# Kernel optimization log

Hardware: AMD Instinct MI355X
Metric: run time of the kernel (lower is better)

The kernel has to match this reference:

```python
import jax, jax.numpy as jnp
import numpy as np

N = 50000      # nodes
E = 800000     # edges (before self loops)
IN = 128       # in_channels
H = 8          # heads
C = 32         # hidden_channels per head
HC = H * C     # 256, concat head dim
G = 256        # number of graphs
NEG_SLOPE = 0.2  # PyG GATConv default


def gat_conv(h_in, src, dst, W, att_s, att_d, bias):
    """PyG-style GATConv, concat heads. src/dst include self loops.
    h_in: [N, F_in]; W: [H*C, F_in]; att_s/att_d: [H, C]; bias: [H*C]."""
    h = (h_in @ W.T).reshape(N, H, C)                      # [N,H,C]
    a_s = jnp.sum(h * att_s, axis=-1)                      # [N,H]
    a_d = jnp.sum(h * att_d, axis=-1)                      # [N,H]
    e = jax.nn.leaky_relu(a_s[src] + a_d[dst], NEG_SLOPE)  # [E',H]
    # segment softmax over incoming edges of each dst node
    m = jax.ops.segment_max(e, dst, num_segments=N)        # [N,H]
    p = jnp.exp(e - m[dst])                                # [E',H]
    denom = jax.ops.segment_sum(p, dst, num_segments=N)    # [N,H]
    alpha = p / denom[dst]                                 # [E',H]
    msg = alpha[:, :, None] * h[src]                       # [E',H,C]
    out = jax.ops.segment_sum(msg, dst, num_segments=N)    # [N,H,C]
    return out.reshape(N, HC) + bias


def setup_inputs() -> dict:
    key = jax.random.key(0)
    ks = jax.random.split(key, 20)
    s = 0.1
    inp = {
        "x": jax.random.normal(ks[0], (N, IN), jnp.float32),
        "edge_index": jax.random.randint(ks[1], (2, E), 0, N, dtype=jnp.int64),
        "batch": jnp.sort(jax.random.randint(ks[2], (N,), 0, G, dtype=jnp.int64)),
        # layer 1: IN -> H*C
        "W1": jax.random.normal(ks[3], (HC, IN), jnp.float32) * s,
        "as1": jax.random.normal(ks[4], (H, C), jnp.float32) * s,
        "ad1": jax.random.normal(ks[5], (H, C), jnp.float32) * s,
        "b1": jnp.zeros((HC,), jnp.float32),
        # layer 2: H*C -> H*C
        "W2": jax.random.normal(ks[6], (HC, HC), jnp.float32) * s,
        "as2": jax.random.normal(ks[7], (H, C), jnp.float32) * s,
        "ad2": jax.random.normal(ks[8], (H, C), jnp.float32) * s,
        "b2": jnp.zeros((HC,), jnp.float32),
        # layer 3: H*C -> H*C
        "W3": jax.random.normal(ks[9], (HC, HC), jnp.float32) * s,
        "as3": jax.random.normal(ks[10], (H, C), jnp.float32) * s,
        "ad3": jax.random.normal(ks[11], (H, C), jnp.float32) * s,
        "b3": jnp.zeros((HC,), jnp.float32),
        # final linear H*C -> 1
        "Wf": jax.random.normal(ks[12], (1, HC), jnp.float32) * s,
        "bf": jnp.zeros((1,), jnp.float32),
    }
    return inp


def reference(x, edge_index, batch, W1, as1, ad1, b1, W2, as2, ad2, b2,
              W3, as3, ad3, b3, Wf, bf):
    # add self loops once (PyG GATConv default add_self_loops=True)
    loop = jnp.arange(N, dtype=edge_index.dtype)
    src = jnp.concatenate([edge_index[0], loop])
    dst = jnp.concatenate([edge_index[1], loop])

    h = jax.nn.relu(gat_conv(x, src, dst, W1, as1, ad1, b1))
    # dropout p=0.01, eval mode -> identity
    h = jax.nn.relu(gat_conv(h, src, dst, W2, as2, ad2, b2))
    h = gat_conv(h, src, dst, W3, as3, ad3, b3)

    # global mean pool per graph
    sums = jax.ops.segment_sum(h, batch, num_segments=G)          # [G,HC]
    cnt = jax.ops.segment_sum(jnp.ones((N, 1), h.dtype), batch, num_segments=G)
    pooled = sums / jnp.maximum(cnt, 1.0)                         # [G,HC]
    return pooled @ Wf.T + bf                                     # [G,1]
```

## Files before the change

kernel.cpp:

```cpp
#include <hip/hip_runtime.h>

#define N_NODES 50000
#define E_EDGES 800000
#define E_EXT   850000
#define IN_CH   128
#define HC      256
#define NHEAD   8
#define CH      32
#define NGRAPH  256
#define SCAN_CHUNK 1024
#define N_CHUNKS ((N_NODES + SCAN_CHUNK - 1) / SCAN_CHUNK)

typedef __bf16 bf16x8 __attribute__((ext_vector_type(8)));
typedef float  f32x4  __attribute__((ext_vector_type(4)));

__device__ inline ushort f2bf(float f) {
    union { float f; unsigned u; } v; v.f = f;
    unsigned u = v.u;
    unsigned r = u + 0x7FFFu + ((u >> 16) & 1u);
    return (ushort)(r >> 16);
}
__device__ inline float bflo(unsigned u) {
    union { unsigned u; float f; } v; v.u = u << 16; return v.f;
}
__device__ inline float bfhi(unsigned u) {
    union { unsigned u; float f; } v; v.u = u & 0xFFFF0000u; return v.f;
}

#define W1_N4 (HC * IN_CH / 4)
#define W23_N4 (HC * HC / 4)
#define CVT_N4 (W1_N4 + 2 * W23_N4)
#define V1_N  (32 * IN_CH)
#define V23_N (32 * HC)
#define COMP_TOT (V1_N + 2 * V23_N)
#define PREP_TOT (CVT_N4 + COMP_TOT + E_EXT)
__global__ __launch_bounds__(256) void prep_kernel(
    const float* __restrict__ W1, const float* __restrict__ W2,
    const float* __restrict__ W3,
    ushort* __restrict__ W1b, ushort* __restrict__ W2b, ushort* __restrict__ W3b,
    const float* __restrict__ as1, const float* __restrict__ ad1,
    const float* __restrict__ as2, const float* __restrict__ ad2,
    const float* __restrict__ as3, const float* __restrict__ ad3,
    const float* __restrict__ b3, const float* __restrict__ Wf,
    float* __restrict__ bw,
    ushort* __restrict__ Vb1, ushort* __restrict__ Vb2, ushort* __restrict__ Vb3,
    const int* __restrict__ ei, int* __restrict__ deg)
{
    int i = blockIdx.x * blockDim.x + threadIdx.x;
    if (blockIdx.x == 0 && threadIdx.x < NHEAD) {
        float s = 0.f;
        for (int c = 0; c < CH; c++)
            s += b3[threadIdx.x * CH + c] * Wf[threadIdx.x * CH + c];
        bw[threadIdx.x] = s;
    }
    if (i < CVT_N4) {
        const float* src; ushort* dst; int k;
        if (i < W1_N4) { src = W1; dst = W1b; k = i; }
        else if (i < W1_N4 + W23_N4) { src = W2; dst = W2b; k = i - W1_N4; }
        else { src = W3; dst = W3b; k = i - W1_N4 - W23_N4; }
        float4 v = *(const float4*)(src + (size_t)k * 4);
        ushort4 o;
        o.x = f2bf(v.x); o.y = f2bf(v.y); o.z = f2bf(v.z); o.w = f2bf(v.w);
        *(ushort4*)(dst + (size_t)k * 4) = o;
        return;
    }
    int c2 = i - CVT_N4;
    if (c2 < COMP_TOT) {
        const float* Wsrc; const float* aw; ushort* dst; int F_, j, k;
        int nrows;
        if (c2 < V1_N) {
            F_ = IN_CH; j = c2 >> 7; k = c2 & 127; Wsrc = W1; dst = Vb1;
            aw = (j < 8) ? as1 : ad1; nrows = 16;
        } else if (c2 < V1_N + V23_N) {
            c2 -= V1_N;
            F_ = HC; j = c2 >> 8; k = c2 & 255; Wsrc = W2; dst = Vb2;
            aw = (j < 8) ? as2 : ad2; nrows = 16;
        } else {
            c2 -= V1_N + V23_N;
            F_ = HC; j = c2 >> 8; k = c2 & 255; Wsrc = W3; dst = Vb3;
            aw = (j < 8) ? as3 : (j < 16 ? Wf : ad3); nrows = 24;
        }
        float v = 0.f;
        if (j < nrows) {
            int h = j & 7;
            for (int c = 0; c < CH; c++)
                v += aw[h * CH + c] * Wsrc[(size_t)(h * CH + c) * F_ + k];
        }
        dst[j * F_ + k] = f2bf(v);
        return;
    }
    int e = i - CVT_N4 - COMP_TOT;
    if (e < E_EXT) {
        int d = (e < E_EDGES) ? ei[E_EDGES + e] : (e - E_EDGES);
        atomicAdd(&deg[d], 1);
    }
}

__global__ __launch_bounds__(256) void mfma_gemm_kernel(
    const ushort* __restrict__ Xb, const float* __restrict__ Xf,
    const ushort* __restrict__ Wb, const ushort* __restrict__ Vb,
    ushort* __restrict__ Hb, int M, int F,
    float* __restrict__ as_out, float* __restrict__ ad_out)
{
    __shared__ ushort As[128][40];
    __shared__ ushort Bs[128][40];
    __shared__ ushort Vs[16][40];
    const int tid  = threadIdx.x;
    const int lane = tid & 63;
    const int wave = tid >> 6;
    const int wr = (wave >> 1) * 64;
    const int wc = (wave & 1) * 64;
    const int bm = blockIdx.x * 128;
    const int bn = blockIdx.y * 128;
    const int lrow = tid >> 2;
    const int lseg = (tid & 3) * 8;
    const int fr = lane & 15;
    const int fk = (lane >> 4) * 8;
    const bool doV = (Vb != nullptr) && (blockIdx.y == 0) && !(wave & 1);

    f32x4 zero = {0.f, 0.f, 0.f, 0.f};
    f32x4 acc[4][4];
    f32x4 accv[4];
    #pragma unroll
    for (int i = 0; i < 4; i++) {
        accv[i] = zero;
        #pragma unroll
        for (int j = 0; j < 4; j++) acc[i][j] = zero;
    }

    for (int k0 = 0; k0 < F; k0 += 32) {
        #pragma unroll
        for (int rr = 0; rr < 2; rr++) {
            int row = lrow + rr * 64;
            int arow = bm + row;
            bf16x8 av = {};
            if (Xf) {
                if (arow < M) {
                    float4 lo = *(const float4*)(Xf + (size_t)arow * F + k0 + lseg);
                    float4 hi = *(const float4*)(Xf + (size_t)arow * F + k0 + lseg + 4);
                    ushort t[8] = { f2bf(lo.x), f2bf(lo.y), f2bf(lo.z), f2bf(lo.w),
                                    f2bf(hi.x), f2bf(hi.y), f2bf(hi.z), f2bf(hi.w) };
                    av = *(const bf16x8*)t;
                }
            } else {
                if (arow < M) av = *(const bf16x8*)(Xb + (size_t)arow * F + k0 + lseg);
            }
            *(bf16x8*)(&As[row][lseg]) = av;
            bf16x8 bv = *(const bf16x8*)(Wb + (size_t)(bn + row) * F + k0 + lseg);
            *(bf16x8*)(&Bs[row][lseg]) = bv;
        }
        if (Vb && tid < 64) {
            int vr = tid >> 2;
            *(bf16x8*)(&Vs[vr][lseg]) = *(const bf16x8*)(Vb + (size_t)vr * F + k0 + lseg);
        }
        __syncthreads();
        bf16x8 a[4], b[4];
        #pragma unroll
        for (int i = 0; i < 4; i++) {
            a[i] = *(const bf16x8*)(&As[wr + i * 16 + fr][fk]);
            b[i] = *(const bf16x8*)(&Bs[wc + i * 16 + fr][fk]);
        }
        #pragma unroll
        for (int i = 0; i < 4; i++)
            #pragma unroll
            for (int j = 0; j < 4; j++)
                acc[i][j] = __builtin_amdgcn_mfma_f32_16x16x32_bf16(
                    a[i], b[j], acc[i][j], 0, 0, 0);
        if (doV) {
            bf16x8 bv = *(const bf16x8*)(&Vs[fr][fk]);
            #pragma unroll
            for (int i = 0; i < 4; i++)
                accv[i] = __builtin_amdgcn_mfma_f32_16x16x32_bf16(
                    a[i], bv, accv[i], 0, 0, 0);
        }
        __syncthreads();
    }
    const int rb = (lane >> 4) * 4;
    #pragma unroll
    for (int i = 0; i < 4; i++) {
        #pragma unroll
        for (int r = 0; r < 4; r++) {
            int m = bm + wr + i * 16 + rb + r;
            if (m < M) {
                #pragma unroll
                for (int j = 0; j < 4; j++)
                    Hb[(size_t)m * HC + bn + wc + j * 16 + fr] = f2bf(acc[i][j][r]);
            }
        }
    }
    if (doV) {
        #pragma unroll
        for (int i = 0; i < 4; i++) {
            #pragma unroll
            for (int r = 0; r < 4; r++) {
                int m = bm + wr + i * 16 + rb + r;
                if (m < M) {
                    float v = accv[i][r];
                    if (fr < 8) as_out[m * NHEAD + fr] = v;
                    else        ad_out[m * NHEAD + fr - 8] = v;
                }
            }
        }
    }
}

__global__ __launch_bounds__(256) void thin_gemm_kernel(
    const ushort* __restrict__ Xb, const ushort* __restrict__ Vb, int M,
    float2* __restrict__ q_out, float* __restrict__ ad_out)
{
    __shared__ ushort As[128][40];
    __shared__ ushort Bs[32][40];
    const int tid  = threadIdx.x;
    const int lane = tid & 63;
    const int wave = tid >> 6;
    const int bm = blockIdx.x * 128;
    const int lrow = tid >> 2;
    const int lseg = (tid & 3) * 8;
    const int fr = lane & 15;
    const int fk = (lane >> 4) * 8;

    f32x4 zero = {0.f, 0.f, 0.f, 0.f};
    f32x4 acc[2][2];
    #pragma unroll
    for (int i = 0; i < 2; i++)
        #pragma unroll
        for (int j = 0; j < 2; j++) acc[i][j] = zero;

    for (int k0 = 0; k0 < HC; k0 += 32) {
        #pragma unroll
        for (int rr = 0; rr < 2; rr++) {
            int row = lrow + rr * 64;
            int arow = bm + row;
            bf16x8 av = {};
            if (arow < M) av = *(const bf16x8*)(Xb + (size_t)arow * HC + k0 + lseg);
            *(bf16x8*)(&As[row][lseg]) = av;
        }
        if (tid < 128) {
            int brow = tid >> 2;
            bf16x8 bv = *(const bf16x8*)(Vb + (size_t)brow * HC + k0 + lseg);
            *(bf16x8*)(&Bs[brow][lseg]) = bv;
        }
        __syncthreads();
        bf16x8 a[2], b[2];
        #pragma unroll
        for (int i = 0; i < 2; i++)
            a[i] = *(const bf16x8*)(&As[wave * 32 + i * 16 + fr][fk]);
        b[0] = *(const bf16x8*)(&Bs[fr][fk]);
        b[1] = *(const bf16x8*)(&Bs[16 + fr][fk]);
        #pragma unroll
        for (int i = 0; i < 2; i++)
            #pragma unroll
            for (int j = 0; j < 2; j++)
                acc[i][j] = __builtin_amdgcn_mfma_f32_16x16x32_bf16(
                    a[i], b[j], acc[i][j], 0, 0, 0);
        __syncthreads();
    }

    const int rb = (lane >> 4) * 4;
    #pragma unroll
    for (int i = 0; i < 2; i++) {
        #pragma unroll
        for (int r = 0; r < 4; r++) {
            int m = bm + wave * 32 + i * 16 + rb + r;
            if (m >= M) continue;
            #pragma unroll
            for (int j = 0; j < 2; j++) {
                int jj = j * 16 + fr;
                float v = acc[i][j][r];
                if (jj < 8)       ((float*)q_out)[(size_t)(m * NHEAD + jj) * 2] = v;
                else if (jj < 16) ((float*)q_out)[(size_t)(m * NHEAD + jj - 8) * 2 + 1] = v;
                else if (jj < 24) ad_out[m * NHEAD + jj - 16] = v;
            }
        }
    }
}

__global__ void scan1_kernel(const int* __restrict__ deg,
                             int* __restrict__ row_ptr, int* __restrict__ csum)
{
    __shared__ int buf[SCAN_CHUNK];
    int t = threadIdx.x;
    int base = blockIdx.x * SCAN_CHUNK;
    int v = (base + t < N_NODES) ? deg[base + t] : 0;
    buf[t] = v;
    __syncthreads();
    for (int off = 1; off < SCAN_CHUNK; off <<= 1) {
        int x = buf[t];
        int y = (t >= off) ? buf[t - off] : 0;
        __syncthreads();
        buf[t] = x + y;
        __syncthreads();
    }
    if (base + t < N_NODES) row_ptr[base + t] = buf[t] - v;
    if (t == SCAN_CHUNK - 1) csum[blockIdx.x] = buf[t];
}

__global__ __launch_bounds__(256) void scan23_kernel(
    int* __restrict__ row_ptr, const int* __restrict__ csum)
{
    __shared__ int pref[64];
    int t = threadIdx.x;
    int i = blockIdx.x * blockDim.x + t;
    if (t < 64) pref[t] = (t < N_CHUNKS) ? csum[t] : 0;
    __syncthreads();
    for (int off = 1; off < 64; off <<= 1) {
        int x = 0, y = 0;
        if (t < 64) { x = pref[t]; y = (t >= off) ? pref[t - off] : 0; }
        __syncthreads();
        if (t < 64) pref[t] = x + y;
        __syncthreads();
    }
    if (i < N_NODES) {
        int ch = i / SCAN_CHUNK;
        row_ptr[i] += (ch > 0) ? pref[ch - 1] : 0;
    }
    if (i == 0) row_ptr[N_NODES] = E_EXT;
}

__global__ __launch_bounds__(256) void scatter_kernel(
    const int* __restrict__ ei, const int* __restrict__ row_ptr,
    int* __restrict__ cur, int* __restrict__ esrc)
{
    int eid = blockIdx.x * blockDim.x + threadIdx.x;
    if (eid >= E_EXT) return;
    int s, d;
    if (eid < E_EDGES) { s = ei[eid]; d = ei[E_EDGES + eid]; }
    else { s = eid - E_EDGES; d = s; }
    int pos = row_ptr[d] + atomicAdd(&cur[d], 1);
    esrc[pos] = s;
}

__global__ __launch_bounds__(256) void gather_kernel(
    const int* __restrict__ row_ptr, const int* __restrict__ esrc,
    const ushort* __restrict__ hb,
    const float* __restrict__ a_s, const float* __restrict__ a_d,
    const float* __restrict__ bias,
    ushort* __restrict__ out_b)
{
    int wv = (blockIdx.x * blockDim.x + threadIdx.x) >> 6;
    int lane = threadIdx.x & 63;
    int half = lane >> 5;
    int lloc = lane & 31;
    int n = wv * 2 + half;
    if (n >= N_NODES) return;
    const int hh = lloc >> 2;
    const int shbase = half << 5;
    const float adv = a_d[n * NHEAD + hh];
    const int beg = row_ptr[n], end = row_ptr[n + 1];

    float a0=0.f,a1=0.f,a2=0.f,a3=0.f,a4=0.f,a5=0.f,a6=0.f,a7=0.f,den=0.f;

    for (int base = beg; base < end; base += 32) {
        int cnt = min(32, end - base);
        int sv = (base + lloc < end) ? esrc[base + lloc] : 0;
        int j = 0;
        for (; j + 4 <= cnt; j += 4) {
            int s0 = __shfl(sv, shbase + j);
            int s1 = __shfl(sv, shbase + j + 1);
            int s2 = __shfl(sv, shbase + j + 2);
            int s3 = __shfl(sv, shbase + j + 3);
            float e0 = a_s[s0 * NHEAD + hh];
            float e1 = a_s[s1 * NHEAD + hh];
            float e2 = a_s[s2 * NHEAD + hh];
            float e3 = a_s[s3 * NHEAD + hh];
            uint4 u0 = *(const uint4*)(hb + (size_t)s0 * HC + lloc * 8);
            uint4 u1 = *(const uint4*)(hb + (size_t)s1 * HC + lloc * 8);
            uint4 u2 = *(const uint4*)(hb + (size_t)s2 * HC + lloc * 8);
            uint4 u3 = *(const uint4*)(hb + (size_t)s3 * HC + lloc * 8);
            e0 += adv; e0 = (e0 > 0.f) ? e0 : 0.2f * e0; float w0 = __expf(e0);
            e1 += adv; e1 = (e1 > 0.f) ? e1 : 0.2f * e1; float w1 = __expf(e1);
            e2 += adv; e2 = (e2 > 0.f) ? e2 : 0.2f * e2; float w2 = __expf(e2);
            e3 += adv; e3 = (e3 > 0.f) ? e3 : 0.2f * e3; float w3 = __expf(e3);
            den += (w0 + w1) + (w2 + w3);
            a0 = fmaf(w0, bflo(u0.x), a0); a1 = fmaf(w0, bfhi(u0.x), a1);
            a2 = fmaf(w0, bflo(u0.y), a2); a3 = fmaf(w0, bfhi(u0.y), a3);
            a4 = fmaf(w0, bflo(u0.z), a4); a5 = fmaf(w0, bfhi(u0.z), a5);
            a6 = fmaf(w0, bflo(u0.w), a6); a7 = fmaf(w0, bfhi(u0.w), a7);
            a0 = fmaf(w1, bflo(u1.x), a0); a1 = fmaf(w1, bfhi(u1.x), a1);
            a2 = fmaf(w1, bflo(u1.y), a2); a3 = fmaf(w1, bfhi(u1.y), a3);
            a4 = fmaf(w1, bflo(u1.z), a4); a5 = fmaf(w1, bfhi(u1.z), a5);
            a6 = fmaf(w1, bflo(u1.w), a6); a7 = fmaf(w1, bfhi(u1.w), a7);
            a0 = fmaf(w2, bflo(u2.x), a0); a1 = fmaf(w2, bfhi(u2.x), a1);
            a2 = fmaf(w2, bflo(u2.y), a2); a3 = fmaf(w2, bfhi(u2.y), a3);
            a4 = fmaf(w2, bflo(u2.z), a4); a5 = fmaf(w2, bfhi(u2.z), a5);
            a6 = fmaf(w2, bflo(u2.w), a6); a7 = fmaf(w2, bfhi(u2.w), a7);
            a0 = fmaf(w3, bflo(u3.x), a0); a1 = fmaf(w3, bfhi(u3.x), a1);
            a2 = fmaf(w3, bflo(u3.y), a2); a3 = fmaf(w3, bfhi(u3.y), a3);
            a4 = fmaf(w3, bflo(u3.z), a4); a5 = fmaf(w3, bfhi(u3.z), a5);
            a6 = fmaf(w3, bflo(u3.w), a6); a7 = fmaf(w3, bfhi(u3.w), a7);
        }
        for (; j < cnt; j++) {
            int s = __shfl(sv, shbase + j);
            float e = a_s[s * NHEAD + hh] + adv;
            e = (e > 0.f) ? e : 0.2f * e;
            float w = __expf(e);
            den += w;
            uint4 u = *(const uint4*)(hb + (size_t)s * HC + lloc * 8);
            a0 = fmaf(w, bflo(u.x), a0); a1 = fmaf(w, bfhi(u.x), a1);
            a2 = fmaf(w, bflo(u.y), a2); a3 = fmaf(w, bfhi(u.y), a3);
            a4 = fmaf(w, bflo(u.z), a4); a5 = fmaf(w, bfhi(u.z), a5);
            a6 = fmaf(w, bflo(u.w), a6); a7 = fmaf(w, bfhi(u.w), a7);
        }
    }
    float inv = 1.f / den;
    float4 ba = *(const float4*)(bias + lloc * 8);
    float4 bb = *(const float4*)(bias + lloc * 8 + 4);
    float o0 = fmaf(a0, inv, ba.x), o1 = fmaf(a1, inv, ba.y);
    float o2 = fmaf(a2, inv, ba.z), o3 = fmaf(a3, inv, ba.w);
    float o4 = fmaf(a4, inv, bb.x), o5 = fmaf(a5, inv, bb.y);
    float o6 = fmaf(a6, inv, bb.z), o7 = fmaf(a7, inv, bb.w);
    o0 = fmaxf(o0, 0.f); o1 = fmaxf(o1, 0.f); o2 = fmaxf(o2, 0.f); o3 = fmaxf(o3, 0.f);
    o4 = fmaxf(o4, 0.f); o5 = fmaxf(o5, 0.f); o6 = fmaxf(o6, 0.f); o7 = fmaxf(o7, 0.f);
    uint4 ob;
    ob.x = (unsigned)f2bf(o0) | ((unsigned)f2bf(o1) << 16);
    ob.y = (unsigned)f2bf(o2) | ((unsigned)f2bf(o3) << 16);
    ob.z = (unsigned)f2bf(o4) | ((unsigned)f2bf(o5) << 16);
    ob.w = (unsigned)f2bf(o6) | ((unsigned)f2bf(o7) << 16);
    *(uint4*)(out_b + (size_t)n * HC + lloc * 8) = ob;
}

__global__ __launch_bounds__(256) void light_gather_kernel(
    const int* __restrict__ row_ptr, const int* __restrict__ esrc,
    const float2* __restrict__ q, const float* __restrict__ a_d,
    const float* __restrict__ bw, float* __restrict__ ndot)
{
    int idx = blockIdx.x * blockDim.x + threadIdx.x;
    if (idx >= N_NODES * NHEAD) return;
    int n = idx >> 3, hh = idx & 7;
    const float adv = a_d[idx];
    const int beg = row_ptr[n], end = row_ptr[n + 1];
    float acc = 0.f, den = 0.f;
    int e = beg;
    for (; e + 4 <= end; e += 4) {
        int s0 = esrc[e], s1 = esrc[e + 1], s2 = esrc[e + 2], s3 = esrc[e + 3];
        float2 q0 = q[s0 * NHEAD + hh];
        float2 q1 = q[s1 * NHEAD + hh];
        float2 q2 = q[s2 * NHEAD + hh];
        float2 q3 = q[s3 * NHEAD + hh];
        float t0 = q0.x + adv; t0 = (t0 > 0.f) ? t0 : 0.2f * t0; float w0 = __expf(t0);
        float t1 = q1.x + adv; t1 = (t1 > 0.f) ? t1 : 0.2f * t1; float w1 = __expf(t1);
        float t2 = q2.x + adv; t2 = (t2 > 0.f) ? t2 : 0.2f * t2; float w2 = __expf(t2);
        float t3 = q3.x + adv; t3 = (t3 > 0.f) ? t3 : 0.2f * t3; float w3 = __expf(t3);
        den += (w0 + w1) + (w2 + w3);
        acc = fmaf(w0, q0.y, acc); acc = fmaf(w1, q1.y, acc);
        acc = fmaf(w2, q2.y, acc); acc = fmaf(w3, q3.y, acc);
    }
    for (; e < end; e++) {
        int s = esrc[e];
        float2 qv = q[s * NHEAD + hh];
        float t = qv.x + adv; t = (t > 0.f) ? t : 0.2f * t;
        float w = __expf(t);
        den += w;
        acc = fmaf(w, qv.y, acc);
    }
    float p = acc / den + bw[hh];
    #pragma unroll
    for (int off = 4; off > 0; off >>= 1) p += __shfl_xor(p, off);
    if (hh == 0) ndot[n] = p;
}

__global__ __launch_bounds__(256) void pool2_kernel(
    const float* __restrict__ ndot, const int* __restrict__ batch,
    const float* __restrict__ bf, float* __restrict__ outp)
{
    __shared__ float red[256];
    int g = blockIdx.x, t = threadIdx.x;
    int lo = 0, hi = N_NODES;
    while (lo < hi) { int mid = (lo + hi) >> 1; if (batch[mid] < g) lo = mid + 1; else hi = mid; }
    int start = lo;
    lo = 0; hi = N_NODES;
    while (lo < hi) { int mid = (lo + hi) >> 1; if (batch[mid] < g + 1) lo = mid + 1; else hi = mid; }
    int end = lo;
    float s = 0.f;
    for (int i = start + t; i < end; i += 256) s += ndot[i];
    red[t] = s;
    __syncthreads();
    for (int k = 128; k > 0; k >>= 1) {
        if (t < k) red[t] += red[t + k];
        __syncthreads();
    }
    if (t == 0) outp[g] = red[0] / fmaxf((float)(end - start), 1.f) + bf[0];
}

extern "C" void kernel_launch(void* const* d_in, const int* in_sizes, int n_in,
                              void* d_out, int out_size, void* d_ws, size_t ws_size,
                              hipStream_t stream)
{
    const float* x    = (const float*)d_in[0];
    const int*   ei   = (const int*)d_in[1];
    const int*   batch= (const int*)d_in[2];
    const float* W1   = (const float*)d_in[3];
    const float* as1  = (const float*)d_in[4];
    const float* ad1  = (const float*)d_in[5];
    const float* b1   = (const float*)d_in[6];
    const float* W2   = (const float*)d_in[7];
    const float* as2  = (const float*)d_in[8];
    const float* ad2  = (const float*)d_in[9];
    const float* b2   = (const float*)d_in[10];
    const float* W3   = (const float*)d_in[11];
    const float* as3  = (const float*)d_in[12];
    const float* ad3  = (const float*)d_in[13];
    const float* b3   = (const float*)d_in[14];
    const float* Wf   = (const float*)d_in[15];
    const float* bf   = (const float*)d_in[16];
    float* out = (float*)d_out;

    char* ws = (char*)d_ws;
    size_t off = 0;
    auto allocb = [&](size_t bytes) {
        void* p = ws + off;
        off += (bytes + 255) & ~(size_t)255;
        return p;
    };
    ushort* bufA    = (ushort*)allocb((size_t)N_NODES * HC * 2);
    ushort* bufB    = (ushort*)allocb((size_t)N_NODES * HC * 2);
    ushort* W1b     = (ushort*)allocb((size_t)HC * IN_CH * 2);
    ushort* W2b     = (ushort*)allocb((size_t)HC * HC * 2);
    ushort* W3b     = (ushort*)allocb((size_t)HC * HC * 2);
    ushort* Vb1     = (ushort*)allocb((size_t)32 * IN_CH * 2);
    ushort* Vb2     = (ushort*)allocb((size_t)32 * HC * 2);
    ushort* Vb3     = (ushort*)allocb((size_t)32 * HC * 2);
    float*  as_buf  = (float*) allocb((size_t)N_NODES * NHEAD * 4);
    float*  ad_buf  = (float*) allocb((size_t)N_NODES * NHEAD * 4);
    float2* q_buf   = (float2*)allocb((size_t)N_NODES * NHEAD * 8);
    float*  bw_buf  = (float*) allocb(NHEAD * 4);
    int*    deg     = (int*)   allocb(N_NODES * 4);
    int*    cur     = (int*)   allocb(N_NODES * 4);
    int*    row_ptr = (int*)   allocb((N_NODES + 1) * 4);
    int*    csum    = (int*)   allocb(64 * 4);
    int*    esrc    = (int*)   allocb(E_EXT * 4);
    float*  ndot    = (float*) allocb(N_NODES * 4);
    (void)ws_size; (void)in_sizes; (void)n_in; (void)out_size;

    const size_t deg_pad = ((size_t)N_NODES * 4 + 255) & ~(size_t)255;
    hipMemsetAsync(deg, 0, deg_pad + (size_t)N_NODES * 4, stream);

    prep_kernel<<<(PREP_TOT + 255) / 256, 256, 0, stream>>>(
        W1, W2, W3, W1b, W2b, W3b,
        as1, ad1, as2, ad2, as3, ad3, b3, Wf, bw_buf,
        Vb1, Vb2, Vb3, ei, deg);

    scan1_kernel<<<N_CHUNKS, SCAN_CHUNK, 0, stream>>>(deg, row_ptr, csum);
    scan23_kernel<<<(N_NODES + 255) / 256, 256, 0, stream>>>(row_ptr, csum);
    scatter_kernel<<<(E_EXT + 255) / 256, 256, 0, stream>>>(ei, row_ptr, cur, esrc);

    dim3 ggrid((N_NODES + 127) / 128, HC / 128);
    const int gather_blocks = (((N_NODES + 1) / 2) * 64 + 255) / 256;
    const int thin_blocks = (N_NODES + 127) / 128;

    mfma_gemm_kernel<<<ggrid, 256, 0, stream>>>(
        nullptr, x, W1b, Vb1, bufB, N_NODES, IN_CH, as_buf, ad_buf);
    gather_kernel<<<gather_blocks, 256, 0, stream>>>(
        row_ptr, esrc, bufB, as_buf, ad_buf, b1, bufA);
    mfma_gemm_kernel<<<ggrid, 256, 0, stream>>>(
        bufA, nullptr, W2b, Vb2, bufB, N_NODES, HC, as_buf, ad_buf);
    gather_kernel<<<gather_blocks, 256, 0, stream>>>(
        row_ptr, esrc, bufB, as_buf, ad_buf, b2, bufA);
    thin_gemm_kernel<<<thin_blocks, 256, 0, stream>>>(
        bufA, Vb3, N_NODES, q_buf, ad_buf);
    light_gather_kernel<<<(N_NODES * NHEAD + 255) / 256, 256, 0, stream>>>(
        row_ptr, esrc, q_buf, ad_buf, bw_buf, ndot);

    pool2_kernel<<<NGRAPH, 256, 0, stream>>>(ndot, batch, bf, out);
}
```

Measured before the change: 310.4 us.

## Fuse layer-3 thin projection into layer-2 gather epilogue, dropping thin GEMM

The layer-3 thin GEMM, which projects node features onto 24 precomputed vectors (attention source, final-linear and attention destination), now runs inside the layer-2 gather epilogue. It uses fp32 V3 vectors and a wave-wide shuffle reduction per output. This skips writing the layer-2 bf16 activations to memory, reading them back, and one kernel launch. In exchange the gather epilogue does 24 dot products with 5 shuffles each per node, which adds ALU and shuffle work to a kernel that is likely bound by memory latency. The prep kernel also stops computing the unused padded V rows.

```diff
diff --git a/kernel.cpp b/kernel.cpp
--- a/kernel.cpp
+++ b/kernel.cpp
@@ -30,9 +30,10 @@
 #define W1_N4 (HC * IN_CH / 4)
 #define W23_N4 (HC * HC / 4)
 #define CVT_N4 (W1_N4 + 2 * W23_N4)
-#define V1_N  (32 * IN_CH)
-#define V23_N (32 * HC)
-#define COMP_TOT (V1_N + 2 * V23_N)
+#define V1_N  (16 * IN_CH)
+#define V2_N  (16 * HC)
+#define V3_N  (24 * HC)
+#define COMP_TOT (V1_N + V2_N + V3_N)
 #define PREP_TOT (CVT_N4 + COMP_TOT + E_EXT)
 __global__ __launch_bounds__(256) void prep_kernel(
     const float* __restrict__ W1, const float* __restrict__ W2,
@@ -43,7 +44,7 @@
     const float* __restrict__ as3, const float* __restrict__ ad3,
     const float* __restrict__ b3, const float* __restrict__ Wf,
     float* __restrict__ bw,
-    ushort* __restrict__ Vb1, ushort* __restrict__ Vb2, ushort* __restrict__ Vb3,
+    ushort* __restrict__ Vb1, ushort* __restrict__ Vb2, float* __restrict__ V3,
     const int* __restrict__ ei, int* __restrict__ deg)
 {
     int i = blockIdx.x * blockDim.x + threadIdx.x;
@@ -65,28 +66,32 @@
         return;
     }
     int c2 = i - CVT_N4;
-    if (c2 < COMP_TOT) {
+    if (c2 < V1_N + V2_N) {
         const float* Wsrc; const float* aw; ushort* dst; int F_, j, k;
-        int nrows;
         if (c2 < V1_N) {
             F_ = IN_CH; j = c2 >> 7; k = c2 & 127; Wsrc = W1; dst = Vb1;
-            aw = (j < 8) ? as1 : ad1; nrows = 16;
-        } else if (c2 < V1_N + V23_N) {
+            aw = (j < 8) ? as1 : ad1;
+        } else {
             c2 -= V1_N;
             F_ = HC; j = c2 >> 8; k = c2 & 255; Wsrc = W2; dst = Vb2;
-            aw = (j < 8) ? as2 : ad2; nrows = 16;
-        } else {
-            c2 -= V1_N + V23_N;
-            F_ = HC; j = c2 >> 8; k = c2 & 255; Wsrc = W3; dst = Vb3;
-            aw = (j < 8) ? as3 : (j < 16 ? Wf : ad3); nrows = 24;
-        }
+            aw = (j < 8) ? as2 : ad2;
+        }
+        int h = j & 7;
         float v = 0.f;
-        if (j < nrows) {
-            int h = j & 7;
-            for (int c = 0; c < CH; c++)
-                v += aw[h * CH + c] * Wsrc[(size_t)(h * CH + c) * F_ + k];
-        }
+        for (int c = 0; c < CH; c++)
+            v += aw[h * CH + c] * Wsrc[(size_t)(h * CH + c) * F_ + k];
         dst[j * F_ + k] = f2bf(v);
+        return;
+    }
+    c2 -= V1_N + V2_N;
+    if (c2 < V3_N) {
+        int j = c2 >> 8, k = c2 & 255;
+        int h = j & 7;
+        const float* aw = (j < 8) ? as3 : (j < 16 ? Wf : ad3);
+        float v = 0.f;
+        for (int c = 0; c < CH; c++)
+            v += aw[h * CH + c] * W3[(size_t)(h * CH + c) * HC + k];
+        V3[j * HC + k] = v;
         return;
     }
     int e = i - CVT_N4 - COMP_TOT;
@@ -116,7 +121,7 @@
     const int lseg = (tid & 3) * 8;
     const int fr = lane & 15;
     const int fk = (lane >> 4) * 8;
-    const bool doV = (Vb != nullptr) && (blockIdx.y == 0) && !(wave & 1);
+    const bool doV = (blockIdx.y == 0) && !(wave & 1);
 
     f32x4 zero = {0.f, 0.f, 0.f, 0.f};
     f32x4 acc[4][4];
@@ -149,7 +154,7 @@
             bf16x8 bv = *(const bf16x8*)(Wb + (size_t)(bn + row) * F + k0 + lseg);
             *(bf16x8*)(&Bs[row][lseg]) = bv;
         }
-        if (Vb && tid < 64) {
+        if (tid < 64) {
             int vr = tid >> 2;
             *(bf16x8*)(&Vs[vr][lseg]) = *(const bf16x8*)(Vb + (size_t)vr * F + k0 + lseg);
         }
@@ -204,77 +209,6 @@
     }
 }
 
-__global__ __launch_bounds__(256) void thin_gemm_kernel(
-    const ushort* __restrict__ Xb, const ushort* __restrict__ Vb, int M,
-    float2* __restrict__ q_out, float* __restrict__ ad_out)
-{
-    __shared__ ushort As[128][40];
-    __shared__ ushort Bs[32][40];
-    const int tid  = threadIdx.x;
-    const int lane = tid & 63;
-    const int wave = tid >> 6;
-    const int bm = blockIdx.x * 128;
-    const int lrow = tid >> 2;
-    const int lseg = (tid & 3) * 8;
-    const int fr = lane & 15;
-    const int fk = (lane >> 4) * 8;
-
-    f32x4 zero = {0.f, 0.f, 0.f, 0.f};
-    f32x4 acc[2][2];
-    #pragma unroll
-    for (int i = 0; i < 2; i++)
-        #pragma unroll
-        for (int j = 0; j < 2; j++) acc[i][j] = zero;
-
-    for (int k0 = 0; k0 < HC; k0 += 32) {
-        #pragma unroll
-        for (int rr = 0; rr < 2; rr++) {
-            int row = lrow + rr * 64;
-            int arow = bm + row;
-            bf16x8 av = {};
-            if (arow < M) av = *(const bf16x8*)(Xb + (size_t)arow * HC + k0 + lseg);
-            *(bf16x8*)(&As[row][lseg]) = av;
-        }
-        if (tid < 128) {
-            int brow = tid >> 2;
-            bf16x8 bv = *(const bf16x8*)(Vb + (size_t)brow * HC + k0 + lseg);
-            *(bf16x8*)(&Bs[brow][lseg]) = bv;
-        }
-        __syncthreads();
-        bf16x8 a[2], b[2];
-        #pragma unroll
-        for (int i = 0; i < 2; i++)
-            a[i] = *(const bf16x8*)(&As[wave * 32 + i * 16 + fr][fk]);
-        b[0] = *(const bf16x8*)(&Bs[fr][fk]);
-        b[1] = *(const bf16x8*)(&Bs[16 + fr][fk]);
-        #pragma unroll
-        for (int i = 0; i < 2; i++)
-            #pragma unroll
-            for (int j = 0; j < 2; j++)
-                acc[i][j] = __builtin_amdgcn_mfma_f32_16x16x32_bf16(
-                    a[i], b[j], acc[i][j], 0, 0, 0);
-        __syncthreads();
-    }
-
-    const int rb = (lane >> 4) * 4;
-    #pragma unroll
-    for (int i = 0; i < 2; i++) {
-        #pragma unroll
-        for (int r = 0; r < 4; r++) {
-            int m = bm + wave * 32 + i * 16 + rb + r;
-            if (m >= M) continue;
-            #pragma unroll
-            for (int j = 0; j < 2; j++) {
-                int jj = j * 16 + fr;
-                float v = acc[i][j][r];
-                if (jj < 8)       ((float*)q_out)[(size_t)(m * NHEAD + jj) * 2] = v;
-                else if (jj < 16) ((float*)q_out)[(size_t)(m * NHEAD + jj - 8) * 2 + 1] = v;
-                else if (jj < 24) ad_out[m * NHEAD + jj - 16] = v;
-            }
-        }
-    }
-}
-
 __global__ void scan1_kernel(const int* __restrict__ deg,
                              int* __restrict__ row_ptr, int* __restrict__ csum)
 {
@@ -335,7 +269,9 @@
     const ushort* __restrict__ hb,
     const float* __restrict__ a_s, const float* __restrict__ a_d,
     const float* __restrict__ bias,
-    ushort* __restrict__ out_b)
+    ushort* __restrict__ out_b,
+    const float* __restrict__ V3,
+    float2* __restrict__ q_out, float* __restrict__ ad3_out)
 {
     int wv = (blockIdx.x * blockDim.x + threadIdx.x) >> 6;
     int lane = threadIdx.x & 63;
@@ -411,12 +347,37 @@
     float o6 = fmaf(a6, inv, bb.z), o7 = fmaf(a7, inv, bb.w);
     o0 = fmaxf(o0, 0.f); o1 = fmaxf(o1, 0.f); o2 = fmaxf(o2, 0.f); o3 = fmaxf(o3, 0.f);
     o4 = fmaxf(o4, 0.f); o5 = fmaxf(o5, 0.f); o6 = fmaxf(o6, 0.f); o7 = fmaxf(o7, 0.f);
-    uint4 ob;
-    ob.x = (unsigned)f2bf(o0) | ((unsigned)f2bf(o1) << 16);
-    ob.y = (unsigned)f2bf(o2) | ((unsigned)f2bf(o3) << 16);
-    ob.z = (unsigned)f2bf(o4) | ((unsigned)f2bf(o5) << 16);
-    ob.w = (unsigned)f2bf(o6) | ((unsigned)f2bf(o7) << 16);
-    *(uint4*)(out_b + (size_t)n * HC + lloc * 8) = ob;
+    if (out_b) {
+        uint4 ob;
+        ob.x = (unsigned)f2bf(o0) | ((unsigned)f2bf(o1) << 16);
+        ob.y = (unsigned)f2bf(o2) | ((unsigned)f2bf(o3) << 16);
+        ob.z = (unsigned)f2bf(o4) | ((unsigned)f2bf(o5) << 16);
+        ob.w = (unsigned)f2bf(o6) | ((unsigned)f2bf(o7) << 16);
+        *(uint4*)(out_b + (size_t)n * HC + lloc * 8) = ob;
+    }
+    if (V3) {
+        float keep = 0.f;
+        #pragma unroll
+        for (int j = 0; j < 24; j++) {
+            const float* vrow = V3 + j * HC + lloc * 8;
+            float4 va = *(const float4*)vrow;
+            float4 vb = *(const float4*)(vrow + 4);
+            float p = o0 * va.x + o1 * va.y + o2 * va.z + o3 * va.w
+                    + o4 * vb.x + o5 * vb.y + o6 * vb.z + o7 * vb.w;
+            p += __shfl_xor(p, 1);
+            p += __shfl_xor(p, 2);
+            p += __shfl_xor(p, 4);
+            p += __shfl_xor(p, 8);
+            p += __shfl_xor(p, 16);
+            if (lloc == j) keep = p;
+        }
+        if (lloc < 8)
+            ((float*)q_out)[(size_t)(n * NHEAD + lloc) * 2] = keep;
+        else if (lloc < 16)
+            ((float*)q_out)[(size_t)(n * NHEAD + lloc - 8) * 2 + 1] = keep;
+        else if (lloc < 24)
+            ad3_out[n * NHEAD + lloc - 16] = keep;
+    }
 }
 
 __global__ __launch_bounds__(256) void light_gather_kernel(
@@ -517,9 +478,9 @@
     ushort* W1b     = (ushort*)allocb((size_t)HC * IN_CH * 2);
     ushort* W2b     = (ushort*)allocb((size_t)HC * HC * 2);
     ushort* W3b     = (ushort*)allocb((size_t)HC * HC * 2);
-    ushort* Vb1     = (ushort*)allocb((size_t)32 * IN_CH * 2);
-    ushort* Vb2     = (ushort*)allocb((size_t)32 * HC * 2);
-    ushort* Vb3     = (ushort*)allocb((size_t)32 * HC * 2);
+    ushort* Vb1     = (ushort*)allocb((size_t)16 * IN_CH * 2);
+    ushort* Vb2     = (ushort*)allocb((size_t)16 * HC * 2);
+    float*  V3f     = (float*) allocb((size_t)24 * HC * 4);
     float*  as_buf  = (float*) allocb((size_t)N_NODES * NHEAD * 4);
     float*  ad_buf  = (float*) allocb((size_t)N_NODES * NHEAD * 4);
     float2* q_buf   = (float2*)allocb((size_t)N_NODES * NHEAD * 8);
@@ -538,7 +499,7 @@
     prep_kernel<<<(PREP_TOT + 255) / 256, 256, 0, stream>>>(
         W1, W2, W3, W1b, W2b, W3b,
         as1, ad1, as2, ad2, as3, ad3, b3, Wf, bw_buf,
-        Vb1, Vb2, Vb3, ei, deg);
+        Vb1, Vb2, V3f, ei, deg);
 
     scan1_kernel<<<N_CHUNKS, SCAN_CHUNK, 0, stream>>>(deg, row_ptr, csum);
     scan23_kernel<<<(N_NODES + 255) / 256, 256, 0, stream>>>(row_ptr, csum);
@@ -546,18 +507,17 @@
 
     dim3 ggrid((N_NODES + 127) / 128, HC / 128);
     const int gather_blocks = (((N_NODES + 1) / 2) * 64 + 255) / 256;
-    const int thin_blocks = (N_NODES + 127) / 128;
 
     mfma_gemm_kernel<<<ggrid, 256, 0, stream>>>(
         nullptr, x, W1b, Vb1, bufB, N_NODES, IN_CH, as_buf, ad_buf);
     gather_kernel<<<gather_blocks, 256, 0, stream>>>(
-        row_ptr, esrc, bufB, as_buf, ad_buf, b1, bufA);
+        row_ptr, esrc, bufB, as_buf, ad_buf, b1, bufA,
+        nullptr, nullptr, nullptr);
     mfma_gemm_kernel<<<ggrid, 256, 0, stream>>>(
         bufA, nullptr, W2b, Vb2, bufB, N_NODES, HC, as_buf, ad_buf);
     gather_kernel<<<gather_blocks, 256, 0, stream>>>(
-        row_ptr, esrc, bufB, as_buf, ad_buf, b2, bufA);
-    thin_gemm_kernel<<<thin_blocks, 256, 0, stream>>>(
-        bufA, Vb3, N_NODES, q_buf, ad_buf);
+        row_ptr, esrc, bufB, as_buf, ad_buf, b2, nullptr,
+        V3f, q_buf, ad_buf);
     light_gather_kernel<<<(N_NODES * NHEAD + 255) / 256, 256, 0, stream>>>(
         row_ptr, esrc, q_buf, ad_buf, bw_buf, ndot);
 
```

After: 313.3 us. No clear change (+0.9%).
